# Optimization experiments

Measured on AMD Instinct MI355X. Metric: run time of the kernel, lower is better.

Reference implementation:

```python
import jax, jax.numpy as jnp
import numpy as np

N_NODES = 100000
N_EDGES = 1600000
IN_CH, HID_CH, OUT_CH = 128, 64, 40


def setup_inputs() -> dict:
    key = jax.random.key(0)
    k_x, k_e, k_w1, k_w2 = jax.random.split(key, 4)
    x = jax.random.normal(k_x, (N_NODES, IN_CH), dtype=jnp.float32)
    edge_index = jax.random.randint(k_e, (2, N_EDGES), 0, N_NODES, dtype=jnp.int64)
    # Glorot-ish scaled weights, zero bias (matches GCNConv init convention)
    W1 = jax.random.normal(k_w1, (IN_CH, HID_CH), dtype=jnp.float32) / np.sqrt(IN_CH)
    b1 = jnp.zeros((HID_CH,), dtype=jnp.float32)
    W2 = jax.random.normal(k_w2, (HID_CH, OUT_CH), dtype=jnp.float32) / np.sqrt(HID_CH)
    b2 = jnp.zeros((OUT_CH,), dtype=jnp.float32)
    return {"x": x, "edge_index": edge_index, "W1": W1, "b1": b1, "W2": W2, "b2": b2}


def _gcn_conv(x, edge_index, W, b, n):
    """GCNConv with normalize=True: linear transform, add self-loops,
    symmetric D^-1/2 A D^-1/2 aggregation (source_to_target flow), bias."""
    h = x @ W  # [n, out]
    loops = jnp.arange(n, dtype=edge_index.dtype)
    row = jnp.concatenate([edge_index[0], loops])  # sources
    col = jnp.concatenate([edge_index[1], loops])  # targets
    deg = jax.ops.segment_sum(jnp.ones_like(col, dtype=h.dtype), col, num_segments=n)
    dinv = jnp.where(deg > 0, jax.lax.rsqrt(deg), jnp.zeros_like(deg))
    w = dinv[row] * dinv[col]  # [E+n] per-edge norm
    out = jax.ops.segment_sum(h[row] * w[:, None], col, num_segments=n)  # scatter-add to targets
    return out + b


def reference(x, edge_index, W1, b1, W2, b2):
    # eval mode: F.dropout(p=0.8, training=False) is identity
    n = x.shape[0]
    h = jax.nn.relu(_gcn_conv(x, edge_index, W1, b1, n))
    return _gcn_conv(h, edge_index, W2, b2, n)  # [N, OUT_CH] logits
```

## Files before the change

kernel.cpp:

```cpp
#include <hip/hip_runtime.h>

#define N_NODES 100000
#define NPAD    100032
#define N_EDGES 1600000
#define IN_CH   128
#define HID_CH  64
#define OUT_CH  40
#define NBKT    196
#define EPB     4096
#define CAP     9216
#define CAPC    10752

using bf16x8 = __attribute__((ext_vector_type(8))) short;
using f32x4  = __attribute__((ext_vector_type(4))) float;

__device__ __forceinline__ float bf2f(unsigned short u) {
    union { unsigned int i; float f; } c; c.i = ((unsigned int)u) << 16; return c.f;
}
__device__ __forceinline__ unsigned short f2bf(float f) {
    union { float f; unsigned int i; } c; c.f = f;
    unsigned int r = c.i + 0x7FFFu + ((c.i >> 16) & 1u);
    return (unsigned short)(r >> 16);
}
__device__ __forceinline__ float4 bf2f4(ushort4 u) {
    return make_float4(bf2f(u.x), bf2f(u.y), bf2f(u.z), bf2f(u.w));
}

__global__ void k_bin(const int* __restrict__ ei, int* __restrict__ gcur,
                      int* __restrict__ ebuf) {
    __shared__ int hist[NBKT];
    __shared__ int lcur[NBKT];
    int tid = threadIdx.x;
    int base = blockIdx.x * EPB;
    int nloc = N_EDGES - base;
    if (nloc > EPB) nloc = EPB;
    int n4 = nloc >> 2;
    const int4* S4 = (const int4*)(ei + base);
    const int4* D4 = (const int4*)(ei + N_EDGES + base);

    if (tid < NBKT) { hist[tid] = 0; }
    __syncthreads();
    for (int i = tid; i < n4; i += 256) {
        int4 d = D4[i];
        atomicAdd(&hist[d.x >> 9], 1);
        atomicAdd(&hist[d.y >> 9], 1);
        atomicAdd(&hist[d.z >> 9], 1);
        atomicAdd(&hist[d.w >> 9], 1);
    }
    __syncthreads();
    if (tid < NBKT) {
        int h = hist[tid];
        lcur[tid] = h ? (tid * CAP + atomicAdd(&gcur[tid], h)) : 0;
    }
    __syncthreads();
    for (int i = tid; i < n4; i += 256) {
        int4 s = S4[i];
        int4 d = D4[i];
        int p;
        p = atomicAdd(&lcur[d.x >> 9], 1); ebuf[p] = s.x | ((d.x & 511) << 17);
        p = atomicAdd(&lcur[d.y >> 9], 1); ebuf[p] = s.y | ((d.y & 511) << 17);
        p = atomicAdd(&lcur[d.z >> 9], 1); ebuf[p] = s.z | ((d.z & 511) << 17);
        p = atomicAdd(&lcur[d.w >> 9], 1); ebuf[p] = s.w | ((d.w & 511) << 17);
    }
}

__global__ void k_node(const int* __restrict__ gcur, const int* __restrict__ ebuf,
                       int* __restrict__ row_start, int* __restrict__ row_end,
                       int* __restrict__ csr_src, float* __restrict__ dinv) {
    __shared__ int cnt[512];
    __shared__ int s[512];
    int tid = threadIdx.x;
    int b = blockIdx.x;
    int node0 = b << 9;
    int lo = b * CAP;
    int lo2 = b * CAPC;
    int hi = lo + gcur[b];
    int n = hi - lo, n4 = n >> 2;
    const int4* E4 = (const int4*)(ebuf + lo);

    cnt[tid] = 0;
    __syncthreads();
    for (int i = tid; i < n4; i += 512) {
        int4 w = E4[i];
        atomicAdd(&cnt[(unsigned)w.x >> 17], 1);
        atomicAdd(&cnt[(unsigned)w.y >> 17], 1);
        atomicAdd(&cnt[(unsigned)w.z >> 17], 1);
        atomicAdd(&cnt[(unsigned)w.w >> 17], 1);
    }
    for (int e = lo + (n4 << 2) + tid; e < hi; e += 512)
        atomicAdd(&cnt[(unsigned)ebuf[e] >> 17], 1);
    __syncthreads();
    int c = cnt[tid];
    int cp = (c + 7) & ~7;
    s[tid] = cp;
    __syncthreads();
#pragma unroll
    for (int off = 1; off < 512; off <<= 1) {
        int tv = (tid >= off) ? s[tid - off] : 0;
        __syncthreads();
        s[tid] += tv;
        __syncthreads();
    }
    int nodestart = lo2 + s[tid] - cp;
    int node = node0 + tid;
    if (node < N_NODES) {
        row_start[node] = nodestart;
        row_end[node]   = nodestart + c;
        dinv[node] = rsqrtf(1.0f + (float)c);
    }
    __syncthreads();
    cnt[tid] = nodestart;
    __syncthreads();
    for (int i = tid; i < n4; i += 512) {
        int4 w = E4[i];
        int p;
        p = atomicAdd(&cnt[(unsigned)w.x >> 17], 1); csr_src[p] = w.x & 0x1FFFF;
        p = atomicAdd(&cnt[(unsigned)w.y >> 17], 1); csr_src[p] = w.y & 0x1FFFF;
        p = atomicAdd(&cnt[(unsigned)w.z >> 17], 1); csr_src[p] = w.z & 0x1FFFF;
        p = atomicAdd(&cnt[(unsigned)w.w >> 17], 1); csr_src[p] = w.w & 0x1FFFF;
    }
    for (int e = lo + (n4 << 2) + tid; e < hi; e += 512) {
        int w = ebuf[e];
        int p = atomicAdd(&cnt[(unsigned)w >> 17], 1);
        csr_src[p] = w & 0x1FFFF;
    }
    for (int p = nodestart + c; p < nodestart + cp; ++p)
        csr_src[p] = N_NODES;
}

__global__ __launch_bounds__(256, 4)
void k_gemm1(const float* __restrict__ x, const float* __restrict__ W1,
             const float* __restrict__ dinv, unsigned short* __restrict__ h1s) {
    __shared__ unsigned short Al[64 * 136];
    __shared__ unsigned short Bl[64 * 136];
    __shared__ float dl[64];
    int tid = threadIdx.x;
    long long node0 = (long long)blockIdx.x * 64;

    const float4* X = (const float4*)x;
    for (int i = tid; i < 64 * 32; i += 256) {
        int r = i >> 5, c4 = i & 31;
        long long gr = node0 + r;
        if (gr >= N_NODES) gr = N_NODES - 1;
        float4 v = X[gr * 32 + c4];
        *(ushort4*)&Al[r * 136 + c4 * 4] =
            make_ushort4(f2bf(v.x), f2bf(v.y), f2bf(v.z), f2bf(v.w));
    }
    for (int i = tid; i < 128 * 64; i += 256) {
        int k = i >> 6, nn = i & 63;
        Bl[nn * 136 + k] = f2bf(W1[i]);
    }
    if (tid < 64) {
        long long gr = node0 + tid;
        dl[tid] = dinv[gr < N_NODES ? gr : N_NODES - 1];
    }
    __syncthreads();

    int lane = tid & 63, wave = tid >> 6;
    int quad = lane >> 4, l16 = lane & 15;
    int arow = wave * 16 + l16;
    f32x4 ac0 = {0,0,0,0}, ac1 = {0,0,0,0}, ac2 = {0,0,0,0}, ac3 = {0,0,0,0};

#pragma unroll
    for (int ks = 0; ks < 4; ++ks) {
        int ko = ks * 32 + quad * 8;
        bf16x8 a  = *(const bf16x8*)&Al[arow * 136 + ko];
        bf16x8 b0 = *(const bf16x8*)&Bl[( 0 + l16) * 136 + ko];
        bf16x8 b1 = *(const bf16x8*)&Bl[(16 + l16) * 136 + ko];
        bf16x8 b2 = *(const bf16x8*)&Bl[(32 + l16) * 136 + ko];
        bf16x8 b3 = *(const bf16x8*)&Bl[(48 + l16) * 136 + ko];
        ac0 = __builtin_amdgcn_mfma_f32_16x16x32_bf16(a, b0, ac0, 0, 0, 0);
        ac1 = __builtin_amdgcn_mfma_f32_16x16x32_bf16(a, b1, ac1, 0, 0, 0);
        ac2 = __builtin_amdgcn_mfma_f32_16x16x32_bf16(a, b2, ac2, 0, 0, 0);
        ac3 = __builtin_amdgcn_mfma_f32_16x16x32_bf16(a, b3, ac3, 0, 0, 0);
    }

#pragma unroll
    for (int r = 0; r < 4; ++r) {
        int rl = wave * 16 + quad * 4 + r;
        long long grow = node0 + rl;
        if (grow < N_NODES) {
            float dd = dl[rl];
            h1s[grow * 64 +  0 + l16] = f2bf(ac0[r] * dd);
            h1s[grow * 64 + 16 + l16] = f2bf(ac1[r] * dd);
            h1s[grow * 64 + 32 + l16] = f2bf(ac2[r] * dd);
            h1s[grow * 64 + 48 + l16] = f2bf(ac3[r] * dd);
        } else {
            h1s[grow * 64 +  0 + l16] = 0;
            h1s[grow * 64 + 16 + l16] = 0;
            h1s[grow * 64 + 32 + l16] = 0;
            h1s[grow * 64 + 48 + l16] = 0;
        }
    }
}

__global__ __launch_bounds__(256, 8)
void k_agg1g2(const int* __restrict__ row_start, const int* __restrict__ row_end,
              const int* __restrict__ csr_src,
              const unsigned short* __restrict__ h1s, const float* __restrict__ dinv,
              const float* __restrict__ b1, const float* __restrict__ W2,
              unsigned short* __restrict__ h2s) {
    __shared__ unsigned short Al[32 * 72];
    __shared__ unsigned short Bl[48 * 72];
    __shared__ float dl[32];
    int tid = threadIdx.x;
    long long node0 = (long long)blockIdx.x * 32;

    for (int i = tid; i < 48 * 64; i += 256) {
        int nn = i >> 6, k = i & 63;
        Bl[nn * 72 + k] = f2bf(nn < OUT_CH ? W2[k * OUT_CH + nn] : 0.0f);
    }
    if (tid < 32) {
        long long gr = node0 + tid;
        dl[tid] = dinv[gr < N_NODES ? gr : N_NODES - 1];
    }
    __syncthreads();

    int cg = tid & 15;
    int nsub = tid >> 4;
    float4 bb = ((const float4*)b1)[cg];
    const ushort4* H = (const ushort4*)h1s;

#pragma unroll
    for (int r4 = 0; r4 < 2; ++r4) {
        int nl = r4 * 16 + nsub;
        long long node = node0 + nl;
        ushort4 res = make_ushort4(0, 0, 0, 0);
        if (node < N_NODES) {
            int e = row_start[node];
            int f = row_end[node];
            int f8 = e + ((f - e + 7) & ~7);
            float4 acc = bf2f4(H[node * 16 + cg]);
            float4 acc2 = {0.f, 0.f, 0.f, 0.f};
            while (e < f8) {
                int s0 = csr_src[e];
                int s1 = csr_src[e + 1];
                int s2 = csr_src[e + 2];
                int s3 = csr_src[e + 3];
                int s4 = csr_src[e + 4];
                int s5 = csr_src[e + 5];
                int s6 = csr_src[e + 6];
                int s7 = csr_src[e + 7];
                float4 v0 = bf2f4(H[(long long)s0 * 16 + cg]);
                float4 v1 = bf2f4(H[(long long)s1 * 16 + cg]);
                float4 v2 = bf2f4(H[(long long)s2 * 16 + cg]);
                float4 v3 = bf2f4(H[(long long)s3 * 16 + cg]);
                float4 u0 = bf2f4(H[(long long)s4 * 16 + cg]);
                float4 u1 = bf2f4(H[(long long)s5 * 16 + cg]);
                float4 u2 = bf2f4(H[(long long)s6 * 16 + cg]);
                float4 u3 = bf2f4(H[(long long)s7 * 16 + cg]);
                acc.x  += (v0.x + v1.x) + (v2.x + v3.x);
                acc.y  += (v0.y + v1.y) + (v2.y + v3.y);
                acc.z  += (v0.z + v1.z) + (v2.z + v3.z);
                acc.w  += (v0.w + v1.w) + (v2.w + v3.w);
                acc2.x += (u0.x + u1.x) + (u2.x + u3.x);
                acc2.y += (u0.y + u1.y) + (u2.y + u3.y);
                acc2.z += (u0.z + u1.z) + (u2.z + u3.z);
                acc2.w += (u0.w + u1.w) + (u2.w + u3.w);
                e += 8;
            }
            acc.x += acc2.x; acc.y += acc2.y; acc.z += acc2.z; acc.w += acc2.w;
            float dd = dl[nl];
            res = make_ushort4(f2bf(fmaxf(acc.x * dd + bb.x, 0.f)),
                               f2bf(fmaxf(acc.y * dd + bb.y, 0.f)),
                               f2bf(fmaxf(acc.z * dd + bb.z, 0.f)),
                               f2bf(fmaxf(acc.w * dd + bb.w, 0.f)));
        }
        *(ushort4*)&Al[nl * 72 + cg * 4] = res;
    }
    __syncthreads();

    int lane = tid & 63, wave = tid >> 6;
    if (wave < 2) {
        int quad = lane >> 4, l16 = lane & 15;
        int arow = wave * 16 + l16;
        f32x4 ac0 = {0,0,0,0}, ac1 = {0,0,0,0}, ac2 = {0,0,0,0};

#pragma unroll
        for (int ks = 0; ks < 2; ++ks) {
            int ko = ks * 32 + quad * 8;
            bf16x8 a  = *(const bf16x8*)&Al[arow * 72 + ko];
            bf16x8 b0 = *(const bf16x8*)&Bl[( 0 + l16) * 72 + ko];
            bf16x8 b1v = *(const bf16x8*)&Bl[(16 + l16) * 72 + ko];
            bf16x8 b2 = *(const bf16x8*)&Bl[(32 + l16) * 72 + ko];
            ac0 = __builtin_amdgcn_mfma_f32_16x16x32_bf16(a, b0, ac0, 0, 0, 0);
            ac1 = __builtin_amdgcn_mfma_f32_16x16x32_bf16(a, b1v, ac1, 0, 0, 0);
            ac2 = __builtin_amdgcn_mfma_f32_16x16x32_bf16(a, b2, ac2, 0, 0, 0);
        }

#pragma unroll
        for (int r = 0; r < 4; ++r) {
            int rl = wave * 16 + quad * 4 + r;
            long long grow = node0 + rl;
            if (grow < N_NODES) {
                float dd = dl[rl];
                h2s[grow * 40 +  0 + l16] = f2bf(ac0[r] * dd);
                h2s[grow * 40 + 16 + l16] = f2bf(ac1[r] * dd);
                if (l16 < 8) h2s[grow * 40 + 32 + l16] = f2bf(ac2[r] * dd);
            } else if (grow < NPAD) {
                h2s[grow * 40 +  0 + l16] = 0;
                h2s[grow * 40 + 16 + l16] = 0;
                if (l16 < 8) h2s[grow * 40 + 32 + l16] = 0;
            }
        }
    }
}

__global__ void k_agg2(const int* __restrict__ row_start, const int* __restrict__ row_end,
                       const int* __restrict__ csr_src,
                       const unsigned short* __restrict__ h2s, const float* __restrict__ dinv,
                       const float* __restrict__ b2, float* __restrict__ out) {
    int idx = blockIdx.x * blockDim.x + threadIdx.x;
    int node = idx >> 4;
    int cg = idx & 15;
    if (node >= N_NODES || cg >= 10) return;
    int e = row_start[node];
    int f = row_end[node];
    int f8 = e + ((f - e + 7) & ~7);
    const ushort4* H = (const ushort4*)h2s;
    float4 acc = bf2f4(H[(long long)node * 10 + cg]);
    float4 acc2 = {0.f, 0.f, 0.f, 0.f};
    while (e < f8) {
        int s0 = csr_src[e];
        int s1 = csr_src[e + 1];
        int s2 = csr_src[e + 2];
        int s3 = csr_src[e + 3];
        int s4 = csr_src[e + 4];
        int s5 = csr_src[e + 5];
        int s6 = csr_src[e + 6];
        int s7 = csr_src[e + 7];
        float4 v0 = bf2f4(H[(long long)s0 * 10 + cg]);
        float4 v1 = bf2f4(H[(long long)s1 * 10 + cg]);
        float4 v2 = bf2f4(H[(long long)s2 * 10 + cg]);
        float4 v3 = bf2f4(H[(long long)s3 * 10 + cg]);
        float4 u0 = bf2f4(H[(long long)s4 * 10 + cg]);
        float4 u1 = bf2f4(H[(long long)s5 * 10 + cg]);
        float4 u2 = bf2f4(H[(long long)s6 * 10 + cg]);
        float4 u3 = bf2f4(H[(long long)s7 * 10 + cg]);
        acc.x  += (v0.x + v1.x) + (v2.x + v3.x);
        acc.y  += (v0.y + v1.y) + (v2.y + v3.y);
        acc.z  += (v0.z + v1.z) + (v2.z + v3.z);
        acc.w  += (v0.w + v1.w) + (v2.w + v3.w);
        acc2.x += (u0.x + u1.x) + (u2.x + u3.x);
        acc2.y += (u0.y + u1.y) + (u2.y + u3.y);
        acc2.z += (u0.z + u1.z) + (u2.z + u3.z);
        acc2.w += (u0.w + u1.w) + (u2.w + u3.w);
        e += 8;
    }
    acc.x += acc2.x; acc.y += acc2.y; acc.z += acc2.z; acc.w += acc2.w;
    float dd = dinv[node];
    float4 b = ((const float4*)b2)[cg];
    acc.x = acc.x * dd + b.x;
    acc.y = acc.y * dd + b.y;
    acc.z = acc.z * dd + b.z;
    acc.w = acc.w * dd + b.w;
    ((float4*)out)[(long long)node * 10 + cg] = acc;
}

extern "C" void kernel_launch(void* const* d_in, const int* in_sizes, int n_in,
                              void* d_out, int out_size, void* d_ws, size_t ws_size,
                              hipStream_t stream) {
    const float* x  = (const float*)d_in[0];
    const int*   ei = (const int*)d_in[1];
    const float* W1 = (const float*)d_in[2];
    const float* b1 = (const float*)d_in[3];
    const float* W2 = (const float*)d_in[4];
    const float* b2 = (const float*)d_in[5];
    float* out = (float*)d_out;

    unsigned short* hbuf  = (unsigned short*)d_ws;
    unsigned short* h2buf = hbuf + 64LL * NPAD;
    int* ebuf      = (int*)(h2buf + 40LL * NPAD);
    int* csr_src   = ebuf + NBKT * CAP;
    int* row_start = csr_src + NBKT * CAPC;
    int* row_end   = row_start + N_NODES;
    int* gcur      = row_end + N_NODES;
    float* dinv    = (float*)(gcur + 256);

    const int B = 256;
    const int g16 = (N_NODES * 16 + B - 1) / B;
    const int gRows = NPAD / 64;
    const int gAgg  = NPAD / 32;

    hipMemsetAsync((void*)gcur, 0, NBKT * sizeof(int), stream);
    k_bin<<<(N_EDGES + EPB - 1) / EPB, B, 0, stream>>>(ei, gcur, ebuf);
    k_node<<<NBKT, 512, 0, stream>>>(gcur, ebuf, row_start, row_end, csr_src, dinv);

    k_gemm1<<<gRows, B, 0, stream>>>(x, W1, dinv, hbuf);
    k_agg1g2<<<gAgg, B, 0, stream>>>(row_start, row_end, csr_src, hbuf, dinv,
                                     b1, W2, h2buf);
    k_agg2<<<g16, B, 0, stream>>>(row_start, row_end, csr_src, h2buf, dinv, b2, out);
}
```

Measured before the change: 220.4 us.

## Widen layer-1 gather to 16-byte rows and load GEMM1 A directly

The layer-1 aggregation now assigns 8 threads per node, each loading 16-byte bf16x8 chunks. Edge indices are fetched cooperatively, one per lane, and broadcast with shuffles, replacing eight redundant index loads per thread and the narrow 8-byte gathers. Each pair of nodes runs for the longer of its two edge lists, padding the shorter one with dummy-node reads. GEMM1 drops its shared-memory staging of x and converts x to bf16 straight from global memory into MFMA operands. Occupancy hint for k_agg1g2 lowered from 8 to 4, and row_start shifted 64 ints, likely so index reads padded past the last bucket stay in bounds.

```diff
diff --git a/kernel.cpp b/kernel.cpp
--- a/kernel.cpp
+++ b/kernel.cpp
@@ -131,21 +131,11 @@
 __global__ __launch_bounds__(256, 4)
 void k_gemm1(const float* __restrict__ x, const float* __restrict__ W1,
              const float* __restrict__ dinv, unsigned short* __restrict__ h1s) {
-    __shared__ unsigned short Al[64 * 136];
     __shared__ unsigned short Bl[64 * 136];
     __shared__ float dl[64];
     int tid = threadIdx.x;
     long long node0 = (long long)blockIdx.x * 64;
 
-    const float4* X = (const float4*)x;
-    for (int i = tid; i < 64 * 32; i += 256) {
-        int r = i >> 5, c4 = i & 31;
-        long long gr = node0 + r;
-        if (gr >= N_NODES) gr = N_NODES - 1;
-        float4 v = X[gr * 32 + c4];
-        *(ushort4*)&Al[r * 136 + c4 * 4] =
-            make_ushort4(f2bf(v.x), f2bf(v.y), f2bf(v.z), f2bf(v.w));
-    }
     for (int i = tid; i < 128 * 64; i += 256) {
         int k = i >> 6, nn = i & 63;
         Bl[nn * 136 + k] = f2bf(W1[i]);
@@ -159,12 +149,21 @@
     int lane = tid & 63, wave = tid >> 6;
     int quad = lane >> 4, l16 = lane & 15;
     int arow = wave * 16 + l16;
+    long long ga = node0 + arow;
+    if (ga >= N_NODES) ga = N_NODES - 1;
+    const float* xr = x + ga * IN_CH;
     f32x4 ac0 = {0,0,0,0}, ac1 = {0,0,0,0}, ac2 = {0,0,0,0}, ac3 = {0,0,0,0};
 
 #pragma unroll
     for (int ks = 0; ks < 4; ++ks) {
         int ko = ks * 32 + quad * 8;
-        bf16x8 a  = *(const bf16x8*)&Al[arow * 136 + ko];
+        float4 xa = *(const float4*)&xr[ko];
+        float4 xb = *(const float4*)&xr[ko + 4];
+        bf16x8 a;
+        a[0] = (short)f2bf(xa.x); a[1] = (short)f2bf(xa.y);
+        a[2] = (short)f2bf(xa.z); a[3] = (short)f2bf(xa.w);
+        a[4] = (short)f2bf(xb.x); a[5] = (short)f2bf(xb.y);
+        a[6] = (short)f2bf(xb.z); a[7] = (short)f2bf(xb.w);
         bf16x8 b0 = *(const bf16x8*)&Bl[( 0 + l16) * 136 + ko];
         bf16x8 b1 = *(const bf16x8*)&Bl[(16 + l16) * 136 + ko];
         bf16x8 b2 = *(const bf16x8*)&Bl[(32 + l16) * 136 + ko];
@@ -194,7 +193,7 @@
     }
 }
 
-__global__ __launch_bounds__(256, 8)
+__global__ __launch_bounds__(256, 4)
 void k_agg1g2(const int* __restrict__ row_start, const int* __restrict__ row_end,
               const int* __restrict__ csr_src,
               const unsigned short* __restrict__ h1s, const float* __restrict__ dinv,
@@ -216,58 +215,74 @@
     }
     __syncthreads();
 
-    int cg = tid & 15;
-    int nsub = tid >> 4;
-    float4 bb = ((const float4*)b1)[cg];
-    const ushort4* H = (const ushort4*)h1s;
-
-#pragma unroll
-    for (int r4 = 0; r4 < 2; ++r4) {
-        int nl = r4 * 16 + nsub;
-        long long node = node0 + nl;
-        ushort4 res = make_ushort4(0, 0, 0, 0);
-        if (node < N_NODES) {
-            int e = row_start[node];
-            int f = row_end[node];
-            int f8 = e + ((f - e + 7) & ~7);
-            float4 acc = bf2f4(H[node * 16 + cg]);
-            float4 acc2 = {0.f, 0.f, 0.f, 0.f};
-            while (e < f8) {
-                int s0 = csr_src[e];
-                int s1 = csr_src[e + 1];
-                int s2 = csr_src[e + 2];
-                int s3 = csr_src[e + 3];
-                int s4 = csr_src[e + 4];
-                int s5 = csr_src[e + 5];
-                int s6 = csr_src[e + 6];
-                int s7 = csr_src[e + 7];
-                float4 v0 = bf2f4(H[(long long)s0 * 16 + cg]);
-                float4 v1 = bf2f4(H[(long long)s1 * 16 + cg]);
-                float4 v2 = bf2f4(H[(long long)s2 * 16 + cg]);
-                float4 v3 = bf2f4(H[(long long)s3 * 16 + cg]);
-                float4 u0 = bf2f4(H[(long long)s4 * 16 + cg]);
-                float4 u1 = bf2f4(H[(long long)s5 * 16 + cg]);
-                float4 u2 = bf2f4(H[(long long)s6 * 16 + cg]);
-                float4 u3 = bf2f4(H[(long long)s7 * 16 + cg]);
-                acc.x  += (v0.x + v1.x) + (v2.x + v3.x);
-                acc.y  += (v0.y + v1.y) + (v2.y + v3.y);
-                acc.z  += (v0.z + v1.z) + (v2.z + v3.z);
-                acc.w  += (v0.w + v1.w) + (v2.w + v3.w);
-                acc2.x += (u0.x + u1.x) + (u2.x + u3.x);
-                acc2.y += (u0.y + u1.y) + (u2.y + u3.y);
-                acc2.z += (u0.z + u1.z) + (u2.z + u3.z);
-                acc2.w += (u0.w + u1.w) + (u2.w + u3.w);
-                e += 8;
-            }
-            acc.x += acc2.x; acc.y += acc2.y; acc.z += acc2.z; acc.w += acc2.w;
-            float dd = dl[nl];
-            res = make_ushort4(f2bf(fmaxf(acc.x * dd + bb.x, 0.f)),
-                               f2bf(fmaxf(acc.y * dd + bb.y, 0.f)),
-                               f2bf(fmaxf(acc.z * dd + bb.z, 0.f)),
-                               f2bf(fmaxf(acc.w * dd + bb.w, 0.f)));
-        }
-        *(ushort4*)&Al[nl * 72 + cg * 4] = res;
-    }
+    int g  = tid >> 4;
+    int hh = (tid >> 3) & 1;
+    int c8 = tid & 7;
+    int nl = g * 2 + hh;
+    long long node = node0 + nl;
+
+    int e0 = 0, d = 0;
+    if (node < N_NODES) { e0 = row_start[node]; d = row_end[node] - e0; }
+    int len8 = (d + 7) & ~7;
+    int lenO = __shfl_xor(len8, 8, 16);
+    int nIt  = (len8 > lenO ? len8 : lenO) >> 3;
+
+    float4 aA = {0.f,0.f,0.f,0.f}, aB = aA, aC = aA, aD = aA;
+
+    int it = 0;
+    while (it < nIt) {
+        bool real = (it << 3) < len8;
+        int base = real ? (e0 + (it << 3)) : e0;
+        int idxr = csr_src[base + c8];
+        int s0 = __shfl(idxr, 0, 8), s1 = __shfl(idxr, 1, 8);
+        int s2 = __shfl(idxr, 2, 8), s3 = __shfl(idxr, 3, 8);
+        int s4 = __shfl(idxr, 4, 8), s5 = __shfl(idxr, 5, 8);
+        int s6 = __shfl(idxr, 6, 8), s7 = __shfl(idxr, 7, 8);
+        if (!real) { s0=s1=s2=s3=s4=s5=s6=s7 = N_NODES; }
+        const unsigned short* Hc = h1s + (long long)c8 * 8;
+        bf16x8 r0 = *(const bf16x8*)&Hc[(long long)s0 * 64];
+        bf16x8 r1 = *(const bf16x8*)&Hc[(long long)s1 * 64];
+        bf16x8 r2 = *(const bf16x8*)&Hc[(long long)s2 * 64];
+        bf16x8 r3 = *(const bf16x8*)&Hc[(long long)s3 * 64];
+        bf16x8 r4 = *(const bf16x8*)&Hc[(long long)s4 * 64];
+        bf16x8 r5 = *(const bf16x8*)&Hc[(long long)s5 * 64];
+        bf16x8 r6 = *(const bf16x8*)&Hc[(long long)s6 * 64];
+        bf16x8 r7 = *(const bf16x8*)&Hc[(long long)s7 * 64];
+#define ACC8(R, LO, HI) { \
+        LO.x += bf2f((unsigned short)R[0]); LO.y += bf2f((unsigned short)R[1]); \
+        LO.z += bf2f((unsigned short)R[2]); LO.w += bf2f((unsigned short)R[3]); \
+        HI.x += bf2f((unsigned short)R[4]); HI.y += bf2f((unsigned short)R[5]); \
+        HI.z += bf2f((unsigned short)R[6]); HI.w += bf2f((unsigned short)R[7]); }
+        ACC8(r0, aA, aB) ACC8(r1, aC, aD)
+        ACC8(r2, aA, aB) ACC8(r3, aC, aD)
+        ACC8(r4, aA, aB) ACC8(r5, aC, aD)
+        ACC8(r6, aA, aB) ACC8(r7, aC, aD)
+#undef ACC8
+        ++it;
+    }
+    aA.x += aC.x; aA.y += aC.y; aA.z += aC.z; aA.w += aC.w;
+    aB.x += aD.x; aB.y += aD.y; aB.z += aD.z; aB.w += aD.w;
+
+    bf16x8 res = {0,0,0,0,0,0,0,0};
+    if (node < N_NODES) {
+        bf16x8 sv = *(const bf16x8*)&h1s[(long long)node * 64 + c8 * 8];
+        aA.x += bf2f((unsigned short)sv[0]); aA.y += bf2f((unsigned short)sv[1]);
+        aA.z += bf2f((unsigned short)sv[2]); aA.w += bf2f((unsigned short)sv[3]);
+        aB.x += bf2f((unsigned short)sv[4]); aB.y += bf2f((unsigned short)sv[5]);
+        aB.z += bf2f((unsigned short)sv[6]); aB.w += bf2f((unsigned short)sv[7]);
+        float dd = dl[nl];
+        float4 blo = ((const float4*)b1)[c8 * 2];
+        float4 bhi = ((const float4*)b1)[c8 * 2 + 1];
+        res[0] = (short)f2bf(fmaxf(aA.x * dd + blo.x, 0.f));
+        res[1] = (short)f2bf(fmaxf(aA.y * dd + blo.y, 0.f));
+        res[2] = (short)f2bf(fmaxf(aA.z * dd + blo.z, 0.f));
+        res[3] = (short)f2bf(fmaxf(aA.w * dd + blo.w, 0.f));
+        res[4] = (short)f2bf(fmaxf(aB.x * dd + bhi.x, 0.f));
+        res[5] = (short)f2bf(fmaxf(aB.y * dd + bhi.y, 0.f));
+        res[6] = (short)f2bf(fmaxf(aB.z * dd + bhi.z, 0.f));
+        res[7] = (short)f2bf(fmaxf(aB.w * dd + bhi.w, 0.f));
+    }
+    *(bf16x8*)&Al[nl * 72 + c8 * 8] = res;
     __syncthreads();
 
     int lane = tid & 63, wave = tid >> 6;
@@ -372,7 +387,7 @@
     unsigned short* h2buf = hbuf + 64LL * NPAD;
     int* ebuf      = (int*)(h2buf + 40LL * NPAD);
     int* csr_src   = ebuf + NBKT * CAP;
-    int* row_start = csr_src + NBKT * CAPC;
+    int* row_start = csr_src + NBKT * CAPC + 64;
     int* row_end   = row_start + N_NODES;
     int* gcur      = row_end + N_NODES;
     float* dinv    = (float*)(gcur + 256);
```

New measurement: 215.8 us. 1.02x faster.
